# Kernel optimization log

Measured on AMD Instinct MI355X. Metric: run time of the kernel, lower is better.

## Reference

```python
import jax, jax.numpy as jnp
import numpy as np

# dims: B batches, N points/batch, S sampled points/batch, M image-projected points/batch,
# V voxels, (H,Wd) range-image size, HID hidden size, NSC scales, NCLS classes
B, N, S, M, V, H, Wd, HID, NSC, NCLS = 2, 120000, 40000, 30000, 100000, 256, 1024, 128, 4, 20


def setup_inputs() -> dict:
    key = jax.random.key(0)
    ks = jax.random.split(key, 24)
    f = jnp.float32
    w = lambda k, shp: (0.02 * jax.random.normal(k, shp, f))
    rows = jax.random.randint(ks[10], (B, M), 0, H, jnp.int32)
    cols = jax.random.randint(ks[11], (B, M), 0, Wd, jnp.int32)
    return {
        "pts_feat_layers": jax.random.normal(ks[0], (NSC, V, HID), f),
        "pts_sample_feat": jax.random.normal(ks[1], (NSC, B * S, HID), f),
        "img_latent_full": jax.random.normal(ks[2], (B, HID, H, Wd), f),
        "img_feat_layers": jax.random.normal(ks[3], (NSC, B * M, HID), f),
        "leaner_W": w(ks[4], (NSC, HID, HID)), "leaner_b": jnp.zeros((NSC, HID), f),
        "fcs1_W": w(ks[5], (NSC, 2 * HID, HID)), "fcs1_b": jnp.zeros((NSC, HID), f),
        "fcs2_W": w(ks[6], (NSC, HID, HID)), "fcs2_b": jnp.zeros((NSC, HID), f),
        "cls_W1": w(ks[7], (NSC * HID, 128)), "cls_b1": jnp.zeros((128,), f),
        "cls_W2": w(ks[8], (128, NCLS)), "cls_b2": jnp.zeros((NCLS,), f),
        "points_img": jnp.stack([rows, cols], axis=-1),              # [B,M,2]
        "point2img_index": jax.random.randint(ks[12], (B, M), 0, N, jnp.int32),
        "sample_index": jax.random.randint(ks[13], (B, S), 0, N, jnp.int32),
        "coors_inv": jax.random.randint(ks[14], (B * N,), 0, V, jnp.int32),
    }


def reference(pts_feat_layers, pts_sample_feat, img_latent_full, img_feat_layers,
              leaner_W, leaner_b, fcs1_W, fcs1_b, fcs2_W, fcs2_b,
              cls_W1, cls_b1, cls_W2, cls_b2,
              points_img, point2img_index, sample_index, coors_inv):
    dt = img_latent_full.dtype
    img_hw = jnp.transpose(img_latent_full, (0, 2, 3, 1))  # [B,H,Wd,HID]
    bar = jnp.arange(B)[:, None]
    # gather image features at projected pixel coords: [B,M,HID]
    img_at_pts = img_hw[bar, points_img[:, :, 0], points_img[:, :, 1]]
    # scatter image features to per-point slots (pts_img_batch_new): [B,N,HID]
    pimg = jax.vmap(lambda idx, v: jnp.zeros((N, HID), dt).at[idx].set(v))(point2img_index, img_at_pts)

    fuse_feats, enc_feats = [], []
    for i in range(NSC):
        # p2img_mapping_spsample: output values depend only on sampled feats + image gather
        sf = pts_sample_feat[i].reshape(B, S, HID)
        sp = jax.vmap(lambda idx, v: jnp.zeros((N, HID), dt).at[idx].set(v))(sample_index, sf)
        sp = sp + pimg  # sample_point_feat == sample_point_feat_f  [B,N,HID]
        # scatter fused point features back into voxel features, then gather per point
        pts_feat = pts_feat_layers[i].at[coors_inv].set(sp.reshape(B * N, HID))
        pts_point = pts_feat[coors_inv].reshape(B, N, HID)
        # p2img_mapping: gather the image-projected points per batch  [B*M,HID]
        pts_g = jnp.take_along_axis(pts_point, point2img_index[:, :, None], axis=1).reshape(B * M, HID)
        fl = jax.nn.relu(pts_g @ leaner_W[i] + leaner_b[i])
        fc = jnp.concatenate([img_feat_layers[i], fl], axis=1) @ fcs1_W[i] + fcs1_b[i]
        fw = jax.nn.sigmoid(fc @ fcs2_W[i] + fcs2_b[i])
        fuse_feats.append(jax.nn.relu(fc * fw))
        enc_feats.append(sp.reshape(B * N, HID))

    seg = jnp.concatenate(fuse_feats, axis=1)                       # [B*M, NSC*HID]
    img_seg_logits = jax.nn.relu(seg @ cls_W1 + cls_b1) @ cls_W2 + cls_b2  # [B*M, NCLS]
    output_3d = jnp.concatenate(enc_feats, axis=1)                  # [B*N, NSC*HID]
    return img_seg_logits, output_3d
```

## Files before the change

### kernel.cpp

```cpp
#include <hip/hip_runtime.h>
#include <hip/hip_bf16.h>
#include <math.h>

#define B_    2
#define N_    120000
#define S_    40000
#define M_    30000
#define V_    100000
#define H_    256
#define WD_   1024
#define HID_  128
#define NSC_  4
#define NCLS_ 20
#define BM_   60000
#define BS_   80000
#define BN_   240000

typedef __attribute__((ext_vector_type(8))) short bfrag8;
typedef __attribute__((ext_vector_type(4))) float facc4;

__device__ __forceinline__ unsigned short f2bf(float f){
  unsigned u = __builtin_bit_cast(unsigned, f);
  u += 0x7fffu + ((u >> 16) & 1u);
  return (unsigned short)(u >> 16);
}
__device__ __forceinline__ float bf2f(unsigned short s){
  return __builtin_bit_cast(float, ((unsigned)s) << 16);
}

__global__ __launch_bounds__(256) void k_winners(const int* __restrict__ p2i,
    const int* __restrict__ si, const int* __restrict__ ci,
    int* __restrict__ win_p, int* __restrict__ win_s, int* __restrict__ win_c){
  int t = blockIdx.x * 256 + threadIdx.x;
  if (t < BM_) atomicMax(&win_p[(t / M_) * N_ + p2i[t]], t);
  if (t < BS_) atomicMax(&win_s[(t / S_) * N_ + si[t]], t);
  if (t < BN_) atomicMax(&win_c[ci[t]], t);
}

__global__ __launch_bounds__(256) void k_gidx(const int* __restrict__ p2i,
    const int* __restrict__ ci, const int* __restrict__ win_c, int* __restrict__ gidx){
  int t = blockIdx.x * 256 + threadIdx.x;
  if (t >= BM_) return;
  int j = (t / M_) * N_ + p2i[t];
  gidx[t] = win_c[ci[j]];
}

__global__ __launch_bounds__(256) void k_imggather(const float* __restrict__ img,
    const int* __restrict__ ptsimg, unsigned short* __restrict__ iap){
  int t = blockIdx.x * 256 + threadIdx.x;
  int row = t >> 7, h = t & 127;
  int b = row / M_;
  int r = ptsimg[row * 2 + 0];
  int c = ptsimg[row * 2 + 1];
  iap[t] = f2bf(img[(((size_t)b * HID_ + h) * H_ + r) * WD_ + c]);
}

__global__ __launch_bounds__(256) void k_out3d(const float* __restrict__ samp,
    const int* __restrict__ win_s, const int* __restrict__ win_p,
    const unsigned short* __restrict__ iap, float* __restrict__ o3d){
  int t = blockIdx.x * 256 + threadIdx.x;
  int j = t >> 5, q = t & 31;
  int sj = win_s[j], pj = win_p[j];
  facc4 iv = {0.f, 0.f, 0.f, 0.f};
  if (pj >= 0){
    ushort4 u = *(const ushort4*)(iap + (size_t)pj * HID_ + q * 4);
    iv.x = bf2f(u.x); iv.y = bf2f(u.y); iv.z = bf2f(u.z); iv.w = bf2f(u.w);
  }
  #pragma unroll
  for (int i = 0; i < NSC_; i++){
    facc4 v = iv;
    if (sj >= 0){
      facc4 s = *(const facc4*)(samp + ((size_t)i * BS_ + sj) * HID_ + q * 4);
      v += s;
    }
    __builtin_nontemporal_store(v, (facc4*)(o3d + (size_t)j * (NSC_ * HID_) + i * HID_ + q * 4));
  }
}

__global__ __launch_bounds__(256) void k_prep(const float* __restrict__ lW,
    const float* __restrict__ f1W, const float* __restrict__ f2W,
    const float* __restrict__ c1W, const float* __restrict__ c2W,
    unsigned short* __restrict__ lwT, unsigned short* __restrict__ f1T,
    unsigned short* __restrict__ f2T, unsigned short* __restrict__ c1T,
    unsigned short* __restrict__ c2T){
  int t = blockIdx.x * 256 + threadIdx.x;
  if (t < 65536){
    int i = t >> 14, r = t & 16383, n = r >> 7, k = r & 127;
    lwT[i * 16384 + n * 128 + k] = f2bf(lW[i * 16384 + k * 128 + n]);
  } else if (t < 196608){
    int e = t - 65536;
    int i = e >> 15, r = e & 32767, n = r >> 8, k = r & 255;
    f1T[i * 32768 + n * 256 + k] = f2bf(f1W[i * 32768 + k * 128 + n]);
  } else if (t < 262144){
    int e = t - 196608;
    int i = e >> 14, r = e & 16383, n = r >> 7, k = r & 127;
    f2T[i * 16384 + n * 128 + k] = f2bf(f2W[i * 16384 + k * 128 + n]);
  } else if (t < 327680){
    int e = t - 262144;
    int n = e >> 9, k = e & 511;
    c1T[n * 512 + k] = f2bf(c1W[k * 128 + n]);
  } else if (t < 330240){
    int e = t - 327680;
    int n = e >> 7, k = e & 127;
    c2T[n * 128 + k] = f2bf(c2W[k * NCLS_ + n]);
  }
}

__global__ __launch_bounds__(256) void k_scale(int i,
    const float* __restrict__ o3d, const int* __restrict__ gidx,
    const float* __restrict__ imgf,
    const unsigned short* __restrict__ lwT, const float* __restrict__ lb,
    const unsigned short* __restrict__ f1T, const float* __restrict__ f1b,
    const unsigned short* __restrict__ f2T, const float* __restrict__ f2b,
    unsigned short* __restrict__ seg){
  __shared__ char lds[81920];
  char* actL = lds + 65536;
  const int lane = threadIdx.x & 63, wv = threadIdx.x >> 6;
  const int rl = lane & 15, kg = lane >> 4;
  const int rowBase = blockIdx.x * 64 + wv * 16;
  const int row = rowBase + rl;
  const bool rv = row < BM_;
  const int lr = wv * 16 + rl;

  {
    const char* src = (const char*)(lwT + (size_t)i * 16384);
    for (int c = threadIdx.x; c < 2048; c += 256){
      int byte = c << 4; int n = byte >> 8;
      *(bfrag8*)(lds + (byte ^ ((n & 7) << 4))) = *(const bfrag8*)(src + byte);
    }
  }
  bfrag8 afr[4];
  {
    const float* aA = o3d + (size_t)(rv ? gidx[row] : 0) * (NSC_ * HID_) + i * HID_;
    #pragma unroll
    for (int kc = 0; kc < 4; kc++){
      int k0 = kc * 32 + kg * 8;
      facc4 s0 = {0,0,0,0}, s1 = {0,0,0,0};
      if (rv){ s0 = *(const facc4*)(aA + k0); s1 = *(const facc4*)(aA + k0 + 4); }
      bfrag8 a;
      a[0]=(short)f2bf(s0.x); a[1]=(short)f2bf(s0.y); a[2]=(short)f2bf(s0.z); a[3]=(short)f2bf(s0.w);
      a[4]=(short)f2bf(s1.x); a[5]=(short)f2bf(s1.y); a[6]=(short)f2bf(s1.z); a[7]=(short)f2bf(s1.w);
      afr[kc] = a;
    }
  }
  __syncthreads();
  facc4 accL[8];
  #pragma unroll
  for (int ct = 0; ct < 8; ct++) accL[ct] = (facc4){0.f,0.f,0.f,0.f};
  #pragma unroll
  for (int kc = 0; kc < 4; kc++){
    int k0 = kc * 32 + kg * 8;
    #pragma unroll
    for (int ct = 0; ct < 8; ct++){
      int col = ct * 16 + rl;
      int byte = (col << 8) + (k0 << 1);
      bfrag8 b = *(const bfrag8*)(lds + (byte ^ ((col & 7) << 4)));
      accL[ct] = __builtin_amdgcn_mfma_f32_16x16x32_bf16(afr[kc], b, accL[ct], 0, 0, 0);
    }
  }
  __syncthreads();
  {
    const float* bias = lb + i * HID_;
    #pragma unroll
    for (int ct = 0; ct < 8; ct++){
      int col = ct * 16 + rl;
      float bv = bias[col];
      #pragma unroll
      for (int r = 0; r < 4; r++){
        int ar = wv * 16 + kg * 4 + r;
        float v = accL[ct][r] + bv; v = v > 0.f ? v : 0.f;
        int byte = ar * 256 + col * 2;
        *(unsigned short*)(actL + (byte ^ ((ar & 7) << 4))) = f2bf(v);
      }
    }
    const char* src = (const char*)(f1T + (size_t)i * 32768);
    for (int c = threadIdx.x; c < 4096; c += 256){
      int byte = c << 4; int n = byte >> 9;
      *(bfrag8*)(lds + (byte ^ ((n & 7) << 4))) = *(const bfrag8*)(src + byte);
    }
  }
  __syncthreads();
  facc4 accF[8];
  #pragma unroll
  for (int ct = 0; ct < 8; ct++) accF[ct] = (facc4){0.f,0.f,0.f,0.f};
  {
    const float* a1 = imgf + ((size_t)i * BM_ + (rv ? row : 0)) * HID_;
    #pragma unroll
    for (int kc = 0; kc < 8; kc++){
      int kk = kc * 32 + kg * 8;
      bfrag8 a;
      if (kc < 4){
        a = (bfrag8){0,0,0,0,0,0,0,0};
        if (rv){
          facc4 s0 = *(const facc4*)(a1 + kk);
          facc4 s1 = *(const facc4*)(a1 + kk + 4);
          a[0]=(short)f2bf(s0.x); a[1]=(short)f2bf(s0.y); a[2]=(short)f2bf(s0.z); a[3]=(short)f2bf(s0.w);
          a[4]=(short)f2bf(s1.x); a[5]=(short)f2bf(s1.y); a[6]=(short)f2bf(s1.z); a[7]=(short)f2bf(s1.w);
        }
      } else {
        int byte = lr * 256 + (kk - 128) * 2;
        a = *(const bfrag8*)(actL + (byte ^ ((lr & 7) << 4)));
      }
      #pragma unroll
      for (int ct = 0; ct < 8; ct++){
        int col = ct * 16 + rl;
        int byte = (col << 9) + (kk << 1);
        bfrag8 b = *(const bfrag8*)(lds + (byte ^ ((col & 7) << 4)));
        accF[ct] = __builtin_amdgcn_mfma_f32_16x16x32_bf16(a, b, accF[ct], 0, 0, 0);
      }
    }
  }
  __syncthreads();
  {
    const float* bias = f1b + i * HID_;
    #pragma unroll
    for (int ct = 0; ct < 8; ct++){
      int col = ct * 16 + rl;
      float bv = bias[col];
      #pragma unroll
      for (int r = 0; r < 4; r++){
        int ar = wv * 16 + kg * 4 + r;
        float v = accF[ct][r] + bv;
        accF[ct][r] = v;
        int byte = ar * 256 + col * 2;
        *(unsigned short*)(actL + (byte ^ ((ar & 7) << 4))) = f2bf(v);
      }
    }
    const char* src = (const char*)(f2T + (size_t)i * 16384);
    for (int c = threadIdx.x; c < 2048; c += 256){
      int byte = c << 4; int n = byte >> 8;
      *(bfrag8*)(lds + (byte ^ ((n & 7) << 4))) = *(const bfrag8*)(src + byte);
    }
  }
  __syncthreads();
  facc4 accT[8];
  #pragma unroll
  for (int ct = 0; ct < 8; ct++) accT[ct] = (facc4){0.f,0.f,0.f,0.f};
  #pragma unroll
  for (int kc = 0; kc < 4; kc++){
    int kk = kc * 32 + kg * 8;
    int byteA = lr * 256 + kk * 2;
    bfrag8 a = *(const bfrag8*)(actL + (byteA ^ ((lr & 7) << 4)));
    #pragma unroll
    for (int ct = 0; ct < 8; ct++){
      int col = ct * 16 + rl;
      int byte = (col << 8) + (kk << 1);
      bfrag8 b = *(const bfrag8*)(lds + (byte ^ ((col & 7) << 4)));
      accT[ct] = __builtin_amdgcn_mfma_f32_16x16x32_bf16(a, b, accT[ct], 0, 0, 0);
    }
  }
  {
    const float* bias2 = f2b + i * HID_;
    #pragma unroll
    for (int ct = 0; ct < 8; ct++){
      int col = ct * 16 + rl;
      float bv2 = bias2[col];
      #pragma unroll
      for (int r = 0; r < 4; r++){
        int orow = rowBase + kg * 4 + r;
        if (orow < BM_){
          float tv = accT[ct][r] + bv2;
          float fw = 1.f / (1.f + expf(-tv));
          float u = accF[ct][r] * fw;
          u = u > 0.f ? u : 0.f;
          seg[(size_t)orow * (NSC_ * HID_) + i * HID_ + col] = f2bf(u);
        }
      }
    }
  }
}

__global__ __launch_bounds__(256) void k_cls(const unsigned short* __restrict__ seg,
    const unsigned short* __restrict__ c1T, const float* __restrict__ c1b,
    const unsigned short* __restrict__ c2T, const float* __restrict__ c2b,
    float* __restrict__ logits){
  __shared__ char lds[81920];
  char* actL = lds + 65536;
  const int lane = threadIdx.x & 63, wv = threadIdx.x >> 6;
  const int rl = lane & 15, kg = lane >> 4;
  const int rowBase = blockIdx.x * 64 + wv * 16;
  const int row = rowBase + rl;
  const bool rv = row < BM_;
  const unsigned short* ar = seg + (size_t)(rv ? row : 0) * 512;
  facc4 acc[8];
  #pragma unroll
  for (int ct = 0; ct < 8; ct++) acc[ct] = (facc4){0.f,0.f,0.f,0.f};
  for (int ph = 0; ph < 2; ph++){
    if (ph) __syncthreads();
    for (int c = threadIdx.x; c < 4096; c += 256){
      int byte = c << 4; int n = byte >> 9; int off = byte & 511;
      *(bfrag8*)(lds + (byte ^ ((n & 7) << 4))) =
          *(const bfrag8*)((const char*)c1T + (size_t)n * 1024 + ph * 512 + off);
    }
    __syncthreads();
    #pragma unroll
    for (int kc = 0; kc < 8; kc++){
      int kk = kc * 32 + kg * 8;
      bfrag8 a = (bfrag8){0,0,0,0,0,0,0,0};
      if (rv) a = *(const bfrag8*)(ar + ph * 256 + kk);
      #pragma unroll
      for (int ct = 0; ct < 8; ct++){
        int col = ct * 16 + rl;
        int byte = (col << 9) + (kk << 1);
        bfrag8 b = *(const bfrag8*)(lds + (byte ^ ((col & 7) << 4)));
        acc[ct] = __builtin_amdgcn_mfma_f32_16x16x32_bf16(a, b, acc[ct], 0, 0, 0);
      }
    }
  }
  __syncthreads();
  #pragma unroll
  for (int ct = 0; ct < 8; ct++){
    int col = ct * 16 + rl;
    float bv = c1b[col];
    #pragma unroll
    for (int r = 0; r < 4; r++){
      int arr = wv * 16 + kg * 4 + r;
      float v = acc[ct][r] + bv; v = v > 0.f ? v : 0.f;
      int byte = arr * 256 + col * 2;
      *(unsigned short*)(actL + (byte ^ ((arr & 7) << 4))) = f2bf(v);
    }
  }
  for (int c = threadIdx.x; c < 320; c += 256)
    *(bfrag8*)(lds + (c << 4)) = *(const bfrag8*)((const char*)c2T + (c << 4));
  __syncthreads();
  {
    int t = threadIdx.x;
    int lrd = t >> 2, n0 = (t & 3) * 5;
    int orow = blockIdx.x * 64 + lrd;
    if (orow < BM_){
      float accD[5];
      #pragma unroll
      for (int q = 0; q < 5; q++) accD[q] = c2b[n0 + q];
      #pragma unroll
      for (int k8 = 0; k8 < 16; k8++){
        int byteA = lrd * 256 + (k8 << 4);
        bfrag8 hv = *(const bfrag8*)(actL + (byteA ^ ((lrd & 7) << 4)));
        #pragma unroll
        for (int q = 0; q < 5; q++){
          bfrag8 w8 = *(const bfrag8*)(lds + (n0 + q) * 256 + (k8 << 4));
          #pragma unroll
          for (int e = 0; e < 8; e++)
            accD[q] += bf2f((unsigned short)hv[e]) * bf2f((unsigned short)w8[e]);
        }
      }
      #pragma unroll
      for (int q = 0; q < 5; q++)
        logits[(size_t)orow * NCLS_ + n0 + q] = accD[q];
    }
  }
}

extern "C" void kernel_launch(void* const* d_in, const int* in_sizes, int n_in,
                              void* d_out, int out_size, void* d_ws, size_t ws_size,
                              hipStream_t stream){
  const float* samp = (const float*)d_in[1];
  const float* img  = (const float*)d_in[2];
  const float* imgf = (const float*)d_in[3];
  const float* lW   = (const float*)d_in[4];
  const float* lb   = (const float*)d_in[5];
  const float* f1W  = (const float*)d_in[6];
  const float* f1b  = (const float*)d_in[7];
  const float* f2W  = (const float*)d_in[8];
  const float* f2b  = (const float*)d_in[9];
  const float* c1W  = (const float*)d_in[10];
  const float* c1b  = (const float*)d_in[11];
  const float* c2W  = (const float*)d_in[12];
  const float* c2b  = (const float*)d_in[13];
  const int* ptsimg = (const int*)d_in[14];
  const int* p2i    = (const int*)d_in[15];
  const int* si     = (const int*)d_in[16];
  const int* ci     = (const int*)d_in[17];

  char* ws = (char*)d_ws;
  int*   win_p = (int*)(ws + 0);
  int*   win_s = (int*)(ws + 960000);
  int*   win_c = (int*)(ws + 1920000);
  int*   gidx  = (int*)(ws + 2320128);
  unsigned short* iap = (unsigned short*)(ws + 2560256);
  unsigned short* seg = (unsigned short*)(ws + 17920384);
  unsigned short* lwT = (unsigned short*)(ws + 79360512);
  unsigned short* f1T = lwT + 65536;
  unsigned short* f2T = f1T + 131072;
  unsigned short* c1T = f2T + 65536;
  unsigned short* c2T = c1T + 65536;

  float* logits = (float*)d_out;
  float* o3d    = (float*)d_out + (size_t)BM_ * NCLS_;

  (void)hipMemsetAsync(ws, 0xFF, 2320000, stream);
  k_winners  <<<938,   256, 0, stream>>>(p2i, si, ci, win_p, win_s, win_c);
  k_imggather<<<30000, 256, 0, stream>>>(img, ptsimg, iap);
  k_gidx     <<<235,   256, 0, stream>>>(p2i, ci, win_c, gidx);
  k_prep     <<<1290,  256, 0, stream>>>(lW, f1W, f2W, c1W, c2W, lwT, f1T, f2T, c1T, c2T);
  k_out3d    <<<30000, 256, 0, stream>>>(samp, win_s, win_p, iap, o3d);
  for (int i = 0; i < NSC_; i++)
    k_scale<<<938, 256, 0, stream>>>(i, o3d, gidx, imgf, lwT, lb, f1T, f1b, f2T, f2b, seg);
  k_cls<<<938, 256, 0, stream>>>(seg, c1T, c1b, c2T, c2b, logits);
}
```

Before: 558.1 us.

## Merge per-scale launches and halve LDS to raise occupancy in scale and classifier kernels

Folds the four per-scale k_scale launches into one grid with the scale index taken from blockIdx, and halves the shared-memory footprint by splitting the 256-wide fcs1 and 512-wide classifier weight staging into 128-wide K chunks with extra barriers. This is meant to let more blocks reside per CU (launch bounds of 3) and to remove launch gaps between scales. It also switches the gathers in k_out3d to nontemporal loads. The cost is extra weight reload passes and synchronisations per block.

```diff
diff --git a/kernel.cpp b/kernel.cpp
--- a/kernel.cpp
+++ b/kernel.cpp
@@ -18,6 +18,7 @@
 
 typedef __attribute__((ext_vector_type(8))) short bfrag8;
 typedef __attribute__((ext_vector_type(4))) float facc4;
+typedef __attribute__((ext_vector_type(4))) unsigned short usvec4;
 
 __device__ __forceinline__ unsigned short f2bf(float f){
   unsigned u = __builtin_bit_cast(unsigned, f);
@@ -63,14 +64,14 @@
   int sj = win_s[j], pj = win_p[j];
   facc4 iv = {0.f, 0.f, 0.f, 0.f};
   if (pj >= 0){
-    ushort4 u = *(const ushort4*)(iap + (size_t)pj * HID_ + q * 4);
+    usvec4 u = __builtin_nontemporal_load((const usvec4*)(iap + (size_t)pj * HID_ + q * 4));
     iv.x = bf2f(u.x); iv.y = bf2f(u.y); iv.z = bf2f(u.z); iv.w = bf2f(u.w);
   }
   #pragma unroll
   for (int i = 0; i < NSC_; i++){
     facc4 v = iv;
     if (sj >= 0){
-      facc4 s = *(const facc4*)(samp + ((size_t)i * BS_ + sj) * HID_ + q * 4);
+      facc4 s = __builtin_nontemporal_load((const facc4*)(samp + ((size_t)i * BS_ + sj) * HID_ + q * 4));
       v += s;
     }
     __builtin_nontemporal_store(v, (facc4*)(o3d + (size_t)j * (NSC_ * HID_) + i * HID_ + q * 4));
@@ -106,18 +107,20 @@
   }
 }
 
-__global__ __launch_bounds__(256) void k_scale(int i,
+__global__ __launch_bounds__(256, 3) void k_scales(
     const float* __restrict__ o3d, const int* __restrict__ gidx,
     const float* __restrict__ imgf,
     const unsigned short* __restrict__ lwT, const float* __restrict__ lb,
     const unsigned short* __restrict__ f1T, const float* __restrict__ f1b,
     const unsigned short* __restrict__ f2T, const float* __restrict__ f2b,
     unsigned short* __restrict__ seg){
-  __shared__ char lds[81920];
-  char* actL = lds + 65536;
+  __shared__ char lds[49152];
+  char* actL = lds + 32768;
+  const int i  = blockIdx.x & 3;
+  const int rb = blockIdx.x >> 2;
   const int lane = threadIdx.x & 63, wv = threadIdx.x >> 6;
   const int rl = lane & 15, kg = lane >> 4;
-  const int rowBase = blockIdx.x * 64 + wv * 16;
+  const int rowBase = rb * 64 + wv * 16;
   const int row = rowBase + rl;
   const bool rv = row < BM_;
   const int lr = wv * 16 + rl;
@@ -174,9 +177,10 @@
       }
     }
     const char* src = (const char*)(f1T + (size_t)i * 32768);
-    for (int c = threadIdx.x; c < 4096; c += 256){
-      int byte = c << 4; int n = byte >> 9;
-      *(bfrag8*)(lds + (byte ^ ((n & 7) << 4))) = *(const bfrag8*)(src + byte);
+    for (int c = threadIdx.x; c < 2048; c += 256){
+      int n = c >> 4, off = (c & 15) << 4;
+      *(bfrag8*)(lds + ((n * 256 + off) ^ ((n & 7) << 4))) =
+          *(const bfrag8*)(src + (size_t)n * 512 + off);
     }
   }
   __syncthreads();
@@ -186,28 +190,45 @@
   {
     const float* a1 = imgf + ((size_t)i * BM_ + (rv ? row : 0)) * HID_;
     #pragma unroll
-    for (int kc = 0; kc < 8; kc++){
+    for (int kc = 0; kc < 4; kc++){
       int kk = kc * 32 + kg * 8;
-      bfrag8 a;
-      if (kc < 4){
-        a = (bfrag8){0,0,0,0,0,0,0,0};
-        if (rv){
-          facc4 s0 = *(const facc4*)(a1 + kk);
-          facc4 s1 = *(const facc4*)(a1 + kk + 4);
-          a[0]=(short)f2bf(s0.x); a[1]=(short)f2bf(s0.y); a[2]=(short)f2bf(s0.z); a[3]=(short)f2bf(s0.w);
-          a[4]=(short)f2bf(s1.x); a[5]=(short)f2bf(s1.y); a[6]=(short)f2bf(s1.z); a[7]=(short)f2bf(s1.w);
-        }
-      } else {
-        int byte = lr * 256 + (kk - 128) * 2;
-        a = *(const bfrag8*)(actL + (byte ^ ((lr & 7) << 4)));
+      bfrag8 a = (bfrag8){0,0,0,0,0,0,0,0};
+      if (rv){
+        facc4 s0 = *(const facc4*)(a1 + kk);
+        facc4 s1 = *(const facc4*)(a1 + kk + 4);
+        a[0]=(short)f2bf(s0.x); a[1]=(short)f2bf(s0.y); a[2]=(short)f2bf(s0.z); a[3]=(short)f2bf(s0.w);
+        a[4]=(short)f2bf(s1.x); a[5]=(short)f2bf(s1.y); a[6]=(short)f2bf(s1.z); a[7]=(short)f2bf(s1.w);
       }
       #pragma unroll
       for (int ct = 0; ct < 8; ct++){
         int col = ct * 16 + rl;
-        int byte = (col << 9) + (kk << 1);
+        int byte = (col << 8) + (kk << 1);
         bfrag8 b = *(const bfrag8*)(lds + (byte ^ ((col & 7) << 4)));
         accF[ct] = __builtin_amdgcn_mfma_f32_16x16x32_bf16(a, b, accF[ct], 0, 0, 0);
       }
+    }
+  }
+  __syncthreads();
+  {
+    const char* src = (const char*)(f1T + (size_t)i * 32768) + 256;
+    for (int c = threadIdx.x; c < 2048; c += 256){
+      int n = c >> 4, off = (c & 15) << 4;
+      *(bfrag8*)(lds + ((n * 256 + off) ^ ((n & 7) << 4))) =
+          *(const bfrag8*)(src + (size_t)n * 512 + off);
+    }
+  }
+  __syncthreads();
+  #pragma unroll
+  for (int kc = 0; kc < 4; kc++){
+    int kl = kc * 32 + kg * 8;
+    int byteA = lr * 256 + kl * 2;
+    bfrag8 a = *(const bfrag8*)(actL + (byteA ^ ((lr & 7) << 4)));
+    #pragma unroll
+    for (int ct = 0; ct < 8; ct++){
+      int col = ct * 16 + rl;
+      int byte = (col << 8) + (kl << 1);
+      bfrag8 b = *(const bfrag8*)(lds + (byte ^ ((col & 7) << 4)));
+      accF[ct] = __builtin_amdgcn_mfma_f32_16x16x32_bf16(a, b, accF[ct], 0, 0, 0);
     }
   }
   __syncthreads();
@@ -270,12 +291,12 @@
   }
 }
 
-__global__ __launch_bounds__(256) void k_cls(const unsigned short* __restrict__ seg,
+__global__ __launch_bounds__(256, 3) void k_cls(const unsigned short* __restrict__ seg,
     const unsigned short* __restrict__ c1T, const float* __restrict__ c1b,
     const unsigned short* __restrict__ c2T, const float* __restrict__ c2b,
     float* __restrict__ logits){
-  __shared__ char lds[81920];
-  char* actL = lds + 65536;
+  __shared__ char lds[49152];
+  char* actL = lds + 32768;
   const int lane = threadIdx.x & 63, wv = threadIdx.x >> 6;
   const int rl = lane & 15, kg = lane >> 4;
   const int rowBase = blockIdx.x * 64 + wv * 16;
@@ -285,23 +306,23 @@
   facc4 acc[8];
   #pragma unroll
   for (int ct = 0; ct < 8; ct++) acc[ct] = (facc4){0.f,0.f,0.f,0.f};
-  for (int ph = 0; ph < 2; ph++){
+  for (int ph = 0; ph < 4; ph++){
     if (ph) __syncthreads();
-    for (int c = threadIdx.x; c < 4096; c += 256){
-      int byte = c << 4; int n = byte >> 9; int off = byte & 511;
-      *(bfrag8*)(lds + (byte ^ ((n & 7) << 4))) =
-          *(const bfrag8*)((const char*)c1T + (size_t)n * 1024 + ph * 512 + off);
+    for (int c = threadIdx.x; c < 2048; c += 256){
+      int n = c >> 4, off = (c & 15) << 4;
+      *(bfrag8*)(lds + ((n * 256 + off) ^ ((n & 7) << 4))) =
+          *(const bfrag8*)((const char*)c1T + (size_t)n * 1024 + ph * 256 + off);
     }
     __syncthreads();
     #pragma unroll
-    for (int kc = 0; kc < 8; kc++){
-      int kk = kc * 32 + kg * 8;
+    for (int kc = 0; kc < 4; kc++){
+      int kl = kc * 32 + kg * 8;
       bfrag8 a = (bfrag8){0,0,0,0,0,0,0,0};
-      if (rv) a = *(const bfrag8*)(ar + ph * 256 + kk);
+      if (rv) a = *(const bfrag8*)(ar + ph * 128 + kl);
       #pragma unroll
       for (int ct = 0; ct < 8; ct++){
         int col = ct * 16 + rl;
-        int byte = (col << 9) + (kk << 1);
+        int byte = (col << 8) + (kl << 1);
         bfrag8 b = *(const bfrag8*)(lds + (byte ^ ((col & 7) << 4)));
         acc[ct] = __builtin_amdgcn_mfma_f32_16x16x32_bf16(a, b, acc[ct], 0, 0, 0);
       }
@@ -393,7 +414,6 @@
   k_gidx     <<<235,   256, 0, stream>>>(p2i, ci, win_c, gidx);
   k_prep     <<<1290,  256, 0, stream>>>(lW, f1W, f2W, c1W, c2W, lwT, f1T, f2T, c1T, c2T);
   k_out3d    <<<30000, 256, 0, stream>>>(samp, win_s, win_p, iap, o3d);
-  for (int i = 0; i < NSC_; i++)
-    k_scale<<<938, 256, 0, stream>>>(i, o3d, gidx, imgf, lwT, lb, f1T, f1b, f2T, f2b, seg);
-  k_cls<<<938, 256, 0, stream>>>(seg, c1T, c1b, c2T, c2b, logits);
-}
+  k_scales   <<<3752,  256, 0, stream>>>(o3d, gidx, imgf, lwT, lb, f1T, f1b, f2T, f2b, seg);
+  k_cls      <<<938,   256, 0, stream>>>(seg, c1T, c1b, c2T, c2b, logits);
+}
```

New measurement: 462.1 us. 17.2% less time.
